# Kernel tuning notes

Hardware: AMD Instinct MI355X
Metric: run time of the kernel (lower is better)

Reference implementation:

```python
import jax, jax.numpy as jnp
import numpy as np

B, S, H = 2, 2048, 1024
NH, G = 16, 4
HD = H // NH          # 64
HPG = NH // G         # 4 heads per kv group


def _xavier(key, fan_in, fan_out):
    limit = np.sqrt(6.0 / (fan_in + fan_out)).astype(np.float32)
    return jax.random.uniform(key, (fan_in, fan_out), jnp.float32, -limit, limit)


def setup_inputs() -> dict:
    key = jax.random.key(0)
    ks = jax.random.split(key, 6)
    hidden_state = jax.random.normal(ks[0], (B, S, H), jnp.float32)
    causal = jnp.tril(jnp.ones((S, S), dtype=bool))
    attention_mask = jnp.broadcast_to(causal, (B, NH, S, S))
    # weights stored as (in, out); torch nn.Linear computes x @ W.T, equivalent math
    Wq = _xavier(ks[1], H, H)
    Wk = _xavier(ks[2], H, G * HD)
    Wv = _xavier(ks[3], H, G * HD)
    Wo = _xavier(ks[4], H, H)
    bq = jnp.zeros((H,), jnp.float32)
    bk = jnp.zeros((G * HD,), jnp.float32)
    bv = jnp.zeros((G * HD,), jnp.float32)
    bo = jnp.zeros((H,), jnp.float32)
    return {"hidden_state": hidden_state, "attention_mask": attention_mask,
            "Wq": Wq, "bq": bq, "Wk": Wk, "bk": bk,
            "Wv": Wv, "bv": bv, "Wo": Wo, "bo": bo}


def reference(hidden_state, attention_mask, Wq, bq, Wk, bk, Wv, bv, Wo, bo):
    b, s, _ = hidden_state.shape
    scale = jnp.float32(1.0 / np.sqrt(HD))
    # projections; query heads split as (group, head_in_group) = head-major order
    q = (hidden_state @ Wq + bq).reshape(b, s, G, HPG, HD)
    k = (hidden_state @ Wk + bk).reshape(b, s, G, HD)
    v = (hidden_state @ Wv + bv).reshape(b, s, G, HD)
    # scores: [b, G, HPG, S, S]  (kv broadcast over heads_per_group, as in torch expand)
    scores = jnp.einsum('bqghd,bkgd->bghqk', q, k) * scale
    mask = attention_mask.reshape(b, G, HPG, s, s)
    scores = jnp.where(mask, scores, -jnp.inf)
    w = jax.nn.softmax(scores, axis=-1)  # dropout=0 (eval): identity
    out = jnp.einsum('bghqk,bkgd->bqghd', w, v).reshape(b, s, H)
    return out @ Wo + bo
```

## Files before the change

### kernel.cpp

```cpp
#include <hip/hip_runtime.h>

#define BATCH 2
#define SEQ   2048
#define HDIM  1024
#define NHEAD 16
#define NGRP  4
#define QKVN  1536
#define MROWS (BATCH*SEQ)

#define DI __device__ __forceinline__

typedef __attribute__((ext_vector_type(4))) float f32x4;
typedef __attribute__((ext_vector_type(8))) __bf16 bf16x8;
typedef __attribute__((ext_vector_type(8))) unsigned short ushort8;
typedef __attribute__((ext_vector_type(4))) unsigned short us4;

DI unsigned short f2bf(float f) {
    unsigned int u = __float_as_uint(f);
    u += 0x7FFF + ((u >> 16) & 1);
    return (unsigned short)(u >> 16);
}

DI bf16x8 u2b(ushort8 u) { union { ushort8 u; bf16x8 b; } x; x.u = u; return x.b; }

DI void async16(const void* g, void* l) {
    __builtin_amdgcn_global_load_lds(
        (const __attribute__((address_space(1))) unsigned int*)g,
        (__attribute__((address_space(3))) unsigned int*)l, 16, 0, 0);
}

#define MFMA16(a, b, c) __builtin_amdgcn_mfma_f32_16x16x32_bf16((a), (b), (c), 0, 0, 0)

__global__ __launch_bounds__(256) void cvt_bf16_kernel(
    const float* __restrict__ in, unsigned short* __restrict__ out, int n8)
{
    int i = blockIdx.x * 256 + threadIdx.x;
    if (i >= n8) return;
    const float4* p = (const float4*)in;
    float4 a = p[i * 2];
    float4 b = p[i * 2 + 1];
    ushort8 r;
    r[0] = f2bf(a.x); r[1] = f2bf(a.y); r[2] = f2bf(a.z); r[3] = f2bf(a.w);
    r[4] = f2bf(b.x); r[5] = f2bf(b.y); r[6] = f2bf(b.z); r[7] = f2bf(b.w);
    *(ushort8*)&out[i * 8] = r;
}

__global__ __launch_bounds__(256) void wtrans_kernel(
    const float* __restrict__ W, unsigned short* __restrict__ Wt, int K, int N)
{
    __shared__ float t[32][33];
    int k0 = blockIdx.y * 32, n0 = blockIdx.x * 32;
    int tx = threadIdx.x & 31, ty = threadIdx.x >> 5;
#pragma unroll
    for (int i = 0; i < 4; ++i)
        t[ty + i * 8][tx] = W[(size_t)(k0 + ty + i * 8) * N + n0 + tx];
    __syncthreads();
#pragma unroll
    for (int i = 0; i < 4; ++i)
        Wt[(size_t)(n0 + ty + i * 8) * K + k0 + tx] = f2bf(t[tx][ty + i * 8]);
}

__global__ void biascat_kernel(const float* __restrict__ bq,
                               const float* __restrict__ bk,
                               const float* __restrict__ bv,
                               float* __restrict__ out)
{
    int i = blockIdx.x * 256 + threadIdx.x;
    if (i < 1024)      out[i] = bq[i];
    else if (i < 1280) out[i] = bk[i - 1024];
    else if (i < 1536) out[i] = bv[i - 1280];
}

template<int MODE>
__global__ __launch_bounds__(256) void gemm_bt(
    const unsigned short* __restrict__ A,
    const unsigned short* __restrict__ Bt,
    const float* __restrict__ bias,
    void* __restrict__ C,
    unsigned short* __restrict__ Kp,
    unsigned short* __restrict__ Vp,
    int M, int N, int K, int ldc)
{
    __shared__ unsigned short Asm[128 * 64];
    __shared__ unsigned short Bsm[128 * 64];
    const int tid = threadIdx.x;
    const int lane = tid & 63;
    const int w = tid >> 6;
    const int l15 = lane & 15;
    const int l4  = lane >> 4;
    const int m0 = blockIdx.y * 128;
    const int n0 = blockIdx.x * 128;
    const int wm = (w >> 1) * 64;
    const int wn = (w & 1) * 64;

    f32x4 acc[4][4] = {};

    const int srow = tid >> 3;
    const int c8   = (tid & 7) * 8;

    for (int kb = 0; kb < K; kb += 64) {
#pragma unroll
        for (int i = 0; i < 4; ++i) {
            int r = srow + i * 32;
            async16(&A[(size_t)(m0 + r) * K + kb + c8], &Asm[r * 64 + c8]);
        }
#pragma unroll
        for (int i = 0; i < 4; ++i) {
            int r = srow + i * 32;
            async16(&Bt[(size_t)(n0 + r) * K + kb + c8], &Bsm[r * 64 + c8]);
        }
        __syncthreads();
#pragma unroll
        for (int kk = 0; kk < 2; ++kk) {
            bf16x8 a[4], b[4];
#pragma unroll
            for (int mi = 0; mi < 4; ++mi)
                a[mi] = *(const bf16x8*)&Asm[(wm + mi * 16 + l15) * 64 + kk * 32 + l4 * 8];
#pragma unroll
            for (int ni = 0; ni < 4; ++ni)
                b[ni] = *(const bf16x8*)&Bsm[(wn + ni * 16 + l15) * 64 + kk * 32 + l4 * 8];
#pragma unroll
            for (int mi = 0; mi < 4; ++mi)
#pragma unroll
                for (int ni = 0; ni < 4; ++ni)
                    acc[mi][ni] = MFMA16(a[mi], b[ni], acc[mi][ni]);
        }
        __syncthreads();
    }

    if (MODE == 0) {
#pragma unroll
        for (int ni = 0; ni < 4; ++ni) {
            int n = n0 + wn + ni * 16 + l15;
            float bv = bias[n];
#pragma unroll
            for (int mi = 0; mi < 4; ++mi) {
                int mrow = m0 + wm + mi * 16 + l4 * 4;
#pragma unroll
                for (int r = 0; r < 4; ++r)
                    ((float*)C)[(size_t)(mrow + r) * ldc + n] = acc[mi][ni][r] + bv;
            }
        }
    } else {
        const int bidx = m0 >> 11;
#pragma unroll
        for (int ni = 0; ni < 4; ++ni) {
            const int nb = n0 + wn + ni * 16;
            const float bv = bias[nb + l15];
            if (nb < 1024) {
#pragma unroll
                for (int mi = 0; mi < 4; ++mi) {
                    int mrow = m0 + wm + mi * 16 + l4 * 4;
#pragma unroll
                    for (int r = 0; r < 4; ++r)
                        ((unsigned short*)C)[(size_t)(mrow + r) * ldc + nb + l15] =
                            f2bf(acc[mi][ni][r] + bv);
                }
            } else if (nb < 1280) {
                const int g  = (nb - 1024) >> 6;
                const int d  = ((nb - 1024) & 63) + l15;
                unsigned short* Kb = Kp + (size_t)(bidx * NGRP + g) * 131072
                                        + (d >> 5) * 512 + (d & 31);
#pragma unroll
                for (int mi = 0; mi < 4; ++mi) {
                    int mrow = m0 + wm + mi * 16 + l4 * 4;
#pragma unroll
                    for (int r = 0; r < 4; ++r) {
                        int s = (mrow + r) & 2047;
                        Kb[(s >> 4) * 1024 + (s & 15) * 32] = f2bf(acc[mi][ni][r] + bv);
                    }
                }
            } else {
                const int g = (nb - 1280) >> 6;
                const int d = ((nb - 1280) & 63) + l15;
                unsigned short* Vb = Vp + (size_t)(bidx * NGRP + g) * 131072 + d * 32;
#pragma unroll
                for (int mi = 0; mi < 4; ++mi) {
                    int srow = (m0 + wm + mi * 16 + l4 * 4) & 2047;
                    us4 u;
#pragma unroll
                    for (int r = 0; r < 4; ++r) u[r] = f2bf(acc[mi][ni][r] + bv);
                    int pos = (((srow & 15) >> 2) * 8) + (((srow >> 4) & 1) * 4);
                    *(us4*)&Vb[(srow >> 5) * 2048 + pos] = u;
                }
            }
        }
    }
}

__global__ __launch_bounds__(256) void flash_gqa(
    const unsigned short* __restrict__ QKV,
    const unsigned short* __restrict__ Kp,
    const unsigned short* __restrict__ Vp,
    unsigned short* __restrict__ O)
{
    const int tid  = threadIdx.x;
    const int lane = tid & 63;
    const int w    = tid >> 6;
    const int l15  = lane & 15;
    const int l4   = lane >> 4;
    const int qb   = blockIdx.x;
    const int h    = blockIdx.y;
    const int b    = blockIdx.z;
    const int g    = h >> 2;
    const int q0   = qb * 64 + w * 16;
    const int q    = q0 + l15;

    const unsigned short* Qb = QKV + (size_t)(b * SEQ) * QKVN + h * 64;
    const unsigned short* Kb = Kp + (size_t)(b * NGRP + g) * 131072;
    const unsigned short* Vb = Vp + (size_t)(b * NGRP + g) * 131072;

    bf16x8 qf[2];
#pragma unroll
    for (int ks = 0; ks < 2; ++ks)
        qf[ks] = *(const bf16x8*)&Qb[(size_t)(q0 + l15) * QKVN + ks * 32 + l4 * 8];

    ushort8 ou;
#pragma unroll
    for (int j = 0; j < 8; ++j) ou[j] = 0x3F80;
    const bf16x8 ones = u2b(ou);

    f32x4 acc[4] = {};
    f32x4 ssum = {0.f, 0.f, 0.f, 0.f};
    float m = -1e30f;
    const float SCL = 0.18033688f;
    const int nkt = qb + 1;

    for (int kt = 0; kt < nkt; ++kt) {
        const int kbase = kt * 64;
        const unsigned short* Kt = Kb + (size_t)(kt * 4) * 1024;
        f32x4 st[4];
#pragma unroll
        for (int t = 0; t < 4; ++t) {
            f32x4 s4 = {0.f, 0.f, 0.f, 0.f};
#pragma unroll
            for (int ks = 0; ks < 2; ++ks) {
                bf16x8 kf = *(const bf16x8*)&Kt[t * 1024 + ks * 512 + l15 * 32 + l4 * 8];
                s4 = MFMA16(kf, qf[ks], s4);
            }
            st[t] = s4;
        }
        const bool diag = (kbase + 63 > q0);
#pragma unroll
        for (int t = 0; t < 4; ++t)
#pragma unroll
            for (int r = 0; r < 4; ++r) {
                float v = st[t][r] * SCL;
                if (diag && (kbase + t * 16 + l4 * 4 + r > q)) v = -1e30f;
                st[t][r] = v;
            }
        float tm = st[0][0];
#pragma unroll
        for (int t = 0; t < 4; ++t)
#pragma unroll
            for (int r = 0; r < 4; ++r) tm = fmaxf(tm, st[t][r]);
        tm = fmaxf(tm, __shfl_xor(tm, 16, 64));
        tm = fmaxf(tm, __shfl_xor(tm, 32, 64));
        const float mn = fmaxf(m, tm);
        const float fr = __builtin_amdgcn_exp2f(m - mn);
        m = mn;
#pragma unroll
        for (int t = 0; t < 4; ++t)
#pragma unroll
            for (int r = 0; r < 4; ++r)
                st[t][r] = __builtin_amdgcn_exp2f(st[t][r] - mn);
        bf16x8 pa0, pa1;
#pragma unroll
        for (int r = 0; r < 4; ++r) {
            pa0[r]     = (__bf16)st[0][r];
            pa0[4 + r] = (__bf16)st[1][r];
            pa1[r]     = (__bf16)st[2][r];
            pa1[4 + r] = (__bf16)st[3][r];
        }
        f32x4 frr;
#pragma unroll
        for (int r = 0; r < 4; ++r) frr[r] = __shfl(fr, l4 * 4 + r, 64);
#pragma unroll
        for (int n = 0; n < 4; ++n)
#pragma unroll
            for (int r = 0; r < 4; ++r) acc[n][r] *= frr[r];
        f32x4 rs = {0.f, 0.f, 0.f, 0.f};
        rs = MFMA16(pa0, ones, rs);
        rs = MFMA16(pa1, ones, rs);
#pragma unroll
        for (int r = 0; r < 4; ++r) ssum[r] = ssum[r] * frr[r] + rs[r];
        const unsigned short* Vt0 = Vb + (size_t)(kt * 2) * 2048;
#pragma unroll
        for (int n = 0; n < 4; ++n) {
#pragma unroll
            for (int s2 = 0; s2 < 2; ++s2) {
                bf16x8 vf = *(const bf16x8*)&Vt0[s2 * 2048 + (n * 16 + l15) * 32 + l4 * 8];
                acc[n] = MFMA16(s2 ? pa1 : pa0, vf, acc[n]);
            }
        }
    }

    f32x4 inv;
#pragma unroll
    for (int r = 0; r < 4; ++r) inv[r] = 1.f / ssum[r];
#pragma unroll
    for (int n = 0; n < 4; ++n)
#pragma unroll
        for (int r = 0; r < 4; ++r)
            O[(size_t)(b * SEQ + q0 + l4 * 4 + r) * HDIM + h * 64 + n * 16 + l15] =
                f2bf(acc[n][r] * inv[r]);
}

extern "C" void kernel_launch(void* const* d_in, const int* in_sizes, int n_in,
                              void* d_out, int out_size, void* d_ws, size_t ws_size,
                              hipStream_t stream)
{
    const float* hidden = (const float*)d_in[0];
    const float* Wq = (const float*)d_in[2];
    const float* bq = (const float*)d_in[3];
    const float* Wk = (const float*)d_in[4];
    const float* bk = (const float*)d_in[5];
    const float* Wv = (const float*)d_in[6];
    const float* bv = (const float*)d_in[7];
    const float* Wo = (const float*)d_in[8];
    const float* bo = (const float*)d_in[9];

    char* ws = (char*)d_ws;
    unsigned short* Xb      = (unsigned short*)(ws);
    unsigned short* QKV     = (unsigned short*)(ws + 8388608);
    unsigned short* WqkvT   = (unsigned short*)(ws + 20971520);
    unsigned short* WoT     = (unsigned short*)(ws + 24117248);
    unsigned short* Kp      = (unsigned short*)(ws + 26214400);
    unsigned short* Vp      = (unsigned short*)(ws + 28311552);
    unsigned short* AttnOut = (unsigned short*)(ws + 30408704);
    float*          bqkv    = (float*)(ws + 38797312);

    cvt_bf16_kernel<<<dim3((MROWS * HDIM) / 8 / 256), 256, 0, stream>>>(hidden, Xb, (MROWS * HDIM) / 8);

    wtrans_kernel<<<dim3(32, 32), 256, 0, stream>>>(Wq, WqkvT,               HDIM, 1024);
    wtrans_kernel<<<dim3( 8, 32), 256, 0, stream>>>(Wk, WqkvT + 1024 * HDIM, HDIM,  256);
    wtrans_kernel<<<dim3( 8, 32), 256, 0, stream>>>(Wv, WqkvT + 1280 * HDIM, HDIM,  256);
    wtrans_kernel<<<dim3(32, 32), 256, 0, stream>>>(Wo, WoT,                 HDIM, 1024);

    biascat_kernel<<<dim3(6), 256, 0, stream>>>(bq, bk, bv, bqkv);

    gemm_bt<1><<<dim3(QKVN / 128, MROWS / 128), 256, 0, stream>>>(
        Xb, WqkvT, bqkv, QKV, Kp, Vp, MROWS, QKVN, HDIM, QKVN);

    flash_gqa<<<dim3(SEQ / 64, NHEAD, BATCH), 256, 0, stream>>>(QKV, Kp, Vp, AttnOut);

    gemm_bt<0><<<dim3(HDIM / 128, MROWS / 128), 256, 0, stream>>>(
        AttnOut, WoT, bo, (float*)d_out, nullptr, nullptr, MROWS, HDIM, HDIM, HDIM);
}
```

Measured before the change: 772.3 us.

## Double-buffer GEMM shared tiles and merge weight-transpose and bias launches

The GEMM now uses two shared-memory buffers per operand, so the async load of the next K tile is issued before the MFMA work on the current tile, overlapping global loads with compute. The three QKV weight transposes are merged into one launch, and the bias-concatenation kernel is removed by passing the three bias pointers straight to the GEMM epilogue. Together these cut launch overhead and memory stalls, at the cost of doubling GEMM shared-memory use (64 KB per block), which may lower occupancy. The loop assumes K is a multiple of 128.

```diff
diff --git a/kernel.cpp b/kernel.cpp
--- a/kernel.cpp
+++ b/kernel.cpp
@@ -45,6 +45,26 @@
     *(ushort8*)&out[i * 8] = r;
 }
 
+__global__ __launch_bounds__(256) void wtrans_qkv_kernel(
+    const float* __restrict__ Wq, const float* __restrict__ Wk,
+    const float* __restrict__ Wv, unsigned short* __restrict__ Wt)
+{
+    __shared__ float t[32][33];
+    int n0 = blockIdx.x * 32, k0 = blockIdx.y * 32;
+    const float* W; int ldw, nn;
+    if (n0 < 1024)      { W = Wq; ldw = 1024; nn = n0; }
+    else if (n0 < 1280) { W = Wk; ldw = 256;  nn = n0 - 1024; }
+    else                { W = Wv; ldw = 256;  nn = n0 - 1280; }
+    int tx = threadIdx.x & 31, ty = threadIdx.x >> 5;
+#pragma unroll
+    for (int i = 0; i < 4; ++i)
+        t[ty + i * 8][tx] = W[(size_t)(k0 + ty + i * 8) * ldw + nn + tx];
+    __syncthreads();
+#pragma unroll
+    for (int i = 0; i < 4; ++i)
+        Wt[(size_t)(n0 + ty + i * 8) * 1024 + k0 + tx] = f2bf(t[tx][ty + i * 8]);
+}
+
 __global__ __launch_bounds__(256) void wtrans_kernel(
     const float* __restrict__ W, unsigned short* __restrict__ Wt, int K, int N)
 {
@@ -58,31 +78,22 @@
 #pragma unroll
     for (int i = 0; i < 4; ++i)
         Wt[(size_t)(n0 + ty + i * 8) * K + k0 + tx] = f2bf(t[tx][ty + i * 8]);
-}
-
-__global__ void biascat_kernel(const float* __restrict__ bq,
-                               const float* __restrict__ bk,
-                               const float* __restrict__ bv,
-                               float* __restrict__ out)
-{
-    int i = blockIdx.x * 256 + threadIdx.x;
-    if (i < 1024)      out[i] = bq[i];
-    else if (i < 1280) out[i] = bk[i - 1024];
-    else if (i < 1536) out[i] = bv[i - 1280];
 }
 
 template<int MODE>
 __global__ __launch_bounds__(256) void gemm_bt(
     const unsigned short* __restrict__ A,
     const unsigned short* __restrict__ Bt,
-    const float* __restrict__ bias,
+    const float* __restrict__ b0,
+    const float* __restrict__ b1,
+    const float* __restrict__ b2,
     void* __restrict__ C,
     unsigned short* __restrict__ Kp,
     unsigned short* __restrict__ Vp,
     int M, int N, int K, int ldc)
 {
-    __shared__ unsigned short Asm[128 * 64];
-    __shared__ unsigned short Bsm[128 * 64];
+    __shared__ unsigned short Asm0[128 * 64], Asm1[128 * 64];
+    __shared__ unsigned short Bsm0[128 * 64], Bsm1[128 * 64];
     const int tid = threadIdx.x;
     const int lane = tid & 63;
     const int w = tid >> 6;
@@ -98,33 +109,44 @@
     const int srow = tid >> 3;
     const int c8   = (tid & 7) * 8;
 
-    for (int kb = 0; kb < K; kb += 64) {
+    auto stage = [&](unsigned short* As, unsigned short* Bs, int kb) {
 #pragma unroll
         for (int i = 0; i < 4; ++i) {
             int r = srow + i * 32;
-            async16(&A[(size_t)(m0 + r) * K + kb + c8], &Asm[r * 64 + c8]);
+            async16(&A[(size_t)(m0 + r) * K + kb + c8], &As[r * 64 + c8]);
         }
 #pragma unroll
         for (int i = 0; i < 4; ++i) {
             int r = srow + i * 32;
-            async16(&Bt[(size_t)(n0 + r) * K + kb + c8], &Bsm[r * 64 + c8]);
-        }
-        __syncthreads();
+            async16(&Bt[(size_t)(n0 + r) * K + kb + c8], &Bs[r * 64 + c8]);
+        }
+    };
+    auto compute = [&](const unsigned short* As, const unsigned short* Bs) {
 #pragma unroll
         for (int kk = 0; kk < 2; ++kk) {
             bf16x8 a[4], b[4];
 #pragma unroll
             for (int mi = 0; mi < 4; ++mi)
-                a[mi] = *(const bf16x8*)&Asm[(wm + mi * 16 + l15) * 64 + kk * 32 + l4 * 8];
+                a[mi] = *(const bf16x8*)&As[(wm + mi * 16 + l15) * 64 + kk * 32 + l4 * 8];
 #pragma unroll
             for (int ni = 0; ni < 4; ++ni)
-                b[ni] = *(const bf16x8*)&Bsm[(wn + ni * 16 + l15) * 64 + kk * 32 + l4 * 8];
+                b[ni] = *(const bf16x8*)&Bs[(wn + ni * 16 + l15) * 64 + kk * 32 + l4 * 8];
 #pragma unroll
             for (int mi = 0; mi < 4; ++mi)
 #pragma unroll
                 for (int ni = 0; ni < 4; ++ni)
                     acc[mi][ni] = MFMA16(a[mi], b[ni], acc[mi][ni]);
         }
+    };
+
+    stage(Asm0, Bsm0, 0);
+    __syncthreads();
+    for (int kb2 = 0; kb2 < K; kb2 += 128) {
+        stage(Asm1, Bsm1, kb2 + 64);
+        compute(Asm0, Bsm0);
+        __syncthreads();
+        if (kb2 + 128 < K) stage(Asm0, Bsm0, kb2 + 128);
+        compute(Asm1, Bsm1);
         __syncthreads();
     }
 
@@ -132,7 +154,7 @@
 #pragma unroll
         for (int ni = 0; ni < 4; ++ni) {
             int n = n0 + wn + ni * 16 + l15;
-            float bv = bias[n];
+            float bv = b0[n];
 #pragma unroll
             for (int mi = 0; mi < 4; ++mi) {
                 int mrow = m0 + wm + mi * 16 + l4 * 4;
@@ -146,8 +168,8 @@
 #pragma unroll
         for (int ni = 0; ni < 4; ++ni) {
             const int nb = n0 + wn + ni * 16;
-            const float bv = bias[nb + l15];
             if (nb < 1024) {
+                const float bv = b0[nb + l15];
 #pragma unroll
                 for (int mi = 0; mi < 4; ++mi) {
                     int mrow = m0 + wm + mi * 16 + l4 * 4;
@@ -157,6 +179,7 @@
                             f2bf(acc[mi][ni][r] + bv);
                 }
             } else if (nb < 1280) {
+                const float bv = b1[nb - 1024 + l15];
                 const int g  = (nb - 1024) >> 6;
                 const int d  = ((nb - 1024) & 63) + l15;
                 unsigned short* Kb = Kp + (size_t)(bidx * NGRP + g) * 131072
@@ -171,17 +194,18 @@
                     }
                 }
             } else {
+                const float bv = b2[nb - 1280 + l15];
                 const int g = (nb - 1280) >> 6;
                 const int d = ((nb - 1280) & 63) + l15;
                 unsigned short* Vb = Vp + (size_t)(bidx * NGRP + g) * 131072 + d * 32;
 #pragma unroll
                 for (int mi = 0; mi < 4; ++mi) {
-                    int srow = (m0 + wm + mi * 16 + l4 * 4) & 2047;
+                    int srow2 = (m0 + wm + mi * 16 + l4 * 4) & 2047;
                     us4 u;
 #pragma unroll
                     for (int r = 0; r < 4; ++r) u[r] = f2bf(acc[mi][ni][r] + bv);
-                    int pos = (((srow & 15) >> 2) * 8) + (((srow >> 4) & 1) * 4);
-                    *(us4*)&Vb[(srow >> 5) * 2048 + pos] = u;
+                    int pos = (((srow2 & 15) >> 2) * 8) + (((srow2 >> 4) & 1) * 4);
+                    *(us4*)&Vb[(srow2 >> 5) * 2048 + pos] = u;
                 }
             }
         }
@@ -328,22 +352,18 @@
     unsigned short* Kp      = (unsigned short*)(ws + 26214400);
     unsigned short* Vp      = (unsigned short*)(ws + 28311552);
     unsigned short* AttnOut = (unsigned short*)(ws + 30408704);
-    float*          bqkv    = (float*)(ws + 38797312);
 
     cvt_bf16_kernel<<<dim3((MROWS * HDIM) / 8 / 256), 256, 0, stream>>>(hidden, Xb, (MROWS * HDIM) / 8);
 
-    wtrans_kernel<<<dim3(32, 32), 256, 0, stream>>>(Wq, WqkvT,               HDIM, 1024);
-    wtrans_kernel<<<dim3( 8, 32), 256, 0, stream>>>(Wk, WqkvT + 1024 * HDIM, HDIM,  256);
-    wtrans_kernel<<<dim3( 8, 32), 256, 0, stream>>>(Wv, WqkvT + 1280 * HDIM, HDIM,  256);
-    wtrans_kernel<<<dim3(32, 32), 256, 0, stream>>>(Wo, WoT,                 HDIM, 1024);
-
-    biascat_kernel<<<dim3(6), 256, 0, stream>>>(bq, bk, bv, bqkv);
+    wtrans_qkv_kernel<<<dim3(48, 32), 256, 0, stream>>>(Wq, Wk, Wv, WqkvT);
+    wtrans_kernel<<<dim3(32, 32), 256, 0, stream>>>(Wo, WoT, HDIM, 1024);
 
     gemm_bt<1><<<dim3(QKVN / 128, MROWS / 128), 256, 0, stream>>>(
-        Xb, WqkvT, bqkv, QKV, Kp, Vp, MROWS, QKVN, HDIM, QKVN);
+        Xb, WqkvT, bq, bk, bv, QKV, Kp, Vp, MROWS, QKVN, HDIM, QKVN);
 
     flash_gqa<<<dim3(SEQ / 64, NHEAD, BATCH), 256, 0, stream>>>(QKV, Kp, Vp, AttnOut);
 
     gemm_bt<0><<<dim3(HDIM / 128, MROWS / 128), 256, 0, stream>>>(
-        AttnOut, WoT, bo, (float*)d_out, nullptr, nullptr, MROWS, HDIM, HDIM, HDIM);
-}
+        AttnOut, WoT, bo, nullptr, nullptr, (float*)d_out, nullptr, nullptr,
+        MROWS, HDIM, HDIM, HDIM);
+}
```

Measured after the change: 760.0 us. No clear change (-1.6%).
